# Performance work log

Hardware: AMD Instinct MI355X
Metric: run time of the kernel (lower is better)

Reference implementation:

```python
import math
import jax, jax.numpy as jnp
import numpy as np

B, S, E, H = 2, 2048, 1024, 16
D = E // H  # head_dim = 64
NEG = jnp.float32(-1e9)  # finite stand-in for masked_fill(-inf) to avoid NaN in attn @ V


def setup_inputs() -> dict:
    key = jax.random.key(0)
    ks = jax.random.split(key, 8)
    inp = {
        "query": jax.random.normal(ks[0], (B, S, E), jnp.float32),
        "key": jax.random.normal(ks[1], (B, S, E), jnp.float32),
        "value": jax.random.normal(ks[2], (B, S, E), jnp.float32),
        "Wq": jax.random.normal(ks[3], (E, E), jnp.float32) * 0.02,
        "bq": jnp.zeros((E,), jnp.float32),
        "Wk": jax.random.normal(ks[4], (E, E), jnp.float32) * 0.02,
        "bk": jnp.zeros((E,), jnp.float32),
        "Wv": jax.random.normal(ks[5], (E, E), jnp.float32) * 0.02,
        "bv": jnp.zeros((E,), jnp.float32),
        "pos_bias": jax.random.normal(ks[6], (H, 2 * S - 1), jnp.float32) * 0.02,
    }
    # gather indices: per-head row index [H,1,1] and relative-position index [S,S]
    inp["idx0"] = jnp.arange(H, dtype=jnp.int32).reshape(H, 1, 1)
    rel = np.arange(S)[:, None] - np.arange(S)[None, :] + (S - 1)  # in [0, 2S-2]
    inp["idx1"] = jnp.asarray(rel, jnp.int32)
    # causal boolean mask: True where masked (j > i)
    inp["mask"] = jnp.triu(jnp.ones((S, S), jnp.bool_), k=1)
    return inp


def _split(x):  # [B,S,E] -> [B,H,S,D]
    return x.reshape(B, S, H, D).transpose(0, 2, 1, 3)


def reference(query, key, value, Wq, bq, Wk, bk, Wv, bv, pos_bias, idx0, idx1, mask):
    q = _split(query @ Wq.T + bq)
    k = _split(key @ Wk.T + bk)
    v = _split(value @ Wv.T + bv)
    logits = jnp.einsum("bhqd,bhkd->bhqk", q, k) / math.sqrt(D)  # [B,H,S,S]
    logits = logits + pos_bias[idx0, idx1]  # gather -> [H,S,S], broadcast over B
    logits = jnp.where(mask, NEG, logits)   # masked_fill
    attn = jax.nn.log_softmax(logits, axis=-1)  # module uses LogSoftmax (faithful)
    out = jnp.einsum("bhqk,bhkd->bhqd", attn, v)
    return out.transpose(0, 2, 1, 3).reshape(B, S, E)
```

## Files before the change

kernel.cpp:

```cpp
#include <hip/hip_runtime.h>
#include <math.h>

constexpr int BB = 2;
constexpr int SS = 2048;
constexpr int EE = 1024;
constexpr int HH = 16;
constexpr int DD = 64;

typedef short short8 __attribute__((ext_vector_type(8)));
typedef short short4_t __attribute__((ext_vector_type(4)));
typedef float floatx4 __attribute__((ext_vector_type(4)));
typedef unsigned short ushort_t;

__device__ __forceinline__ ushort_t f2bf(float f) {
    unsigned int u = __float_as_uint(f);
    u += 0x7fffu + ((u >> 16) & 1u);
    return (ushort_t)(u >> 16);
}
__device__ __forceinline__ float bf2f(short s) {
    return __uint_as_float(((unsigned)(ushort_t)s) << 16);
}

__device__ __forceinline__ void gl_lds16(const void* g, void* l) {
    __builtin_amdgcn_global_load_lds(
        (const __attribute__((address_space(1))) void*)g,
        (__attribute__((address_space(3))) void*)l, 16, 0, 0);
}

__global__ __launch_bounds__(256) void repack_all(
    const float* __restrict__ x0, const float* __restrict__ x1, const float* __restrict__ x2,
    const float* __restrict__ w0, const float* __restrict__ w1, const float* __restrict__ w2,
    ushort_t* __restrict__ Xbf, ushort_t* __restrict__ Wbf)
{
    const int idx = blockIdx.x * 256 + threadIdx.x;
    const int row = idx >> 7;
    const int gir = idx & 127;
    const float* src;
    ushort_t* dst;
    int r;
    if (row < 3 * BB * SS) {
        const int z = row >> 12; r = row & (BB * SS - 1);
        src = (z == 0) ? x0 : (z == 1) ? x1 : x2;
        dst = Xbf + (size_t)z * BB * SS * EE;
    } else {
        const int rw = row - 3 * BB * SS;
        const int z = rw >> 10; r = rw & (EE - 1);
        src = (z == 0) ? w0 : (z == 1) ? w1 : w2;
        dst = Wbf + (size_t)z * EE * EE;
    }
    const int blk = gir >> 3, g = gir & 7;
    const int gp = g ^ (r & 7);
    const float* sp = src + (size_t)r * EE + gir * 8;
    float4 a = *(const float4*)sp;
    float4 b = *(const float4*)(sp + 4);
    short8 o;
    o[0] = (short)f2bf(a.x); o[1] = (short)f2bf(a.y); o[2] = (short)f2bf(a.z); o[3] = (short)f2bf(a.w);
    o[4] = (short)f2bf(b.x); o[5] = (short)f2bf(b.y); o[6] = (short)f2bf(b.z); o[7] = (short)f2bf(b.w);
    *(short8*)&dst[(size_t)r * EE + blk * 64 + gp * 8] = o;
}

__global__ __launch_bounds__(256) void proj_kernel(
    const ushort_t* __restrict__ Xall, const ushort_t* __restrict__ Wall,
    const float* __restrict__ bq, const float* __restrict__ bk, const float* __restrict__ bv,
    ushort_t* __restrict__ qb, ushort_t* __restrict__ kbb, ushort_t* __restrict__ vtb)
{
    __shared__ __align__(16) ushort_t Xs[128 * 64];
    __shared__ __align__(16) ushort_t Ws[128 * 64];

    const int z = blockIdx.z;
    const ushort_t* X = Xall + (size_t)z * BB * SS * EE;
    const ushort_t* W = Wall + (size_t)z * EE * EE;
    const float* bias = (z == 0) ? bq : (z == 1) ? bk : bv;

    const int t = threadIdx.x, w = t >> 6, l = t & 63, ln = t & 15, qd = (t >> 4) & 3;
    const int row0 = blockIdx.x * 128;
    const int col0 = blockIdx.y * 128;
    const int wzm = (w & 1) * 64, wzn = (w >> 1) * 64;

    floatx4 acc[4][4];
    #pragma unroll
    for (int i = 0; i < 4; ++i)
        #pragma unroll
        for (int j = 0; j < 4; ++j)
            acc[i][j] = (floatx4){0.f, 0.f, 0.f, 0.f};

    for (int k0 = 0; k0 < EE; k0 += 64) {
        __syncthreads();
        #pragma unroll
        for (int j = 0; j < 4; ++j) {
            const int c = w * 4 + j;
            const int r = c * 8 + (l >> 3);
            gl_lds16(&X[(size_t)(row0 + r) * EE + k0 + (l & 7) * 8], &Xs[c * 512]);
            gl_lds16(&W[(size_t)(col0 + r) * EE + k0 + (l & 7) * 8], &Ws[c * 512]);
        }
        __syncthreads();

        const ushort_t* Am = (z < 2) ? Ws : Xs;
        const ushort_t* Bn = (z < 2) ? Xs : Ws;
        #pragma unroll
        for (int kh = 0; kh < 2; ++kh) {
            const int sw = ((kh * 4 + qd) ^ (ln & 7)) * 8;
            short8 af[4], bfr[4];
            #pragma unroll
            for (int mi = 0; mi < 4; ++mi)
                af[mi] = *(const short8*)&Am[(wzm + mi * 16 + ln) * 64 + sw];
            #pragma unroll
            for (int ni = 0; ni < 4; ++ni)
                bfr[ni] = *(const short8*)&Bn[(wzn + ni * 16 + ln) * 64 + sw];
            #pragma unroll
            for (int mi = 0; mi < 4; ++mi)
                #pragma unroll
                for (int ni = 0; ni < 4; ++ni)
                    acc[mi][ni] = __builtin_amdgcn_mfma_f32_16x16x32_bf16(af[mi], bfr[ni], acc[mi][ni], 0, 0, 0);
        }
    }

    if (z < 2) {
        ushort_t* dst = z ? kbb : qb;
        #pragma unroll
        for (int mi = 0; mi < 4; ++mi) {
            const int o0 = col0 + wzm + mi * 16 + qd * 4;
            const float4 b4 = *(const float4*)&bias[o0];
            const int h = o0 >> 6, d0 = o0 & 63;
            const int g = d0 >> 3, dlow = d0 & 7;
            #pragma unroll
            for (int ni = 0; ni < 4; ++ni) {
                const int s = row0 + wzn + ni * 16 + ln;
                const int b = s >> 11, sr = s & (SS - 1);
                const int gp = g ^ (sr & 7);
                short4_t pk;
                pk[0] = (short)f2bf(acc[mi][ni][0] + b4.x);
                pk[1] = (short)f2bf(acc[mi][ni][1] + b4.y);
                pk[2] = (short)f2bf(acc[mi][ni][2] + b4.z);
                pk[3] = (short)f2bf(acc[mi][ni][3] + b4.w);
                *(short4_t*)&dst[((size_t)((b * HH + h) * SS) + sr) * DD + gp * 8 + dlow] = pk;
            }
        }
    } else {
        #pragma unroll
        for (int mi = 0; mi < 4; ++mi) {
            const int s0 = row0 + wzm + mi * 16 + qd * 4;
            const int b = s0 >> 11, sr0 = s0 & (SS - 1);
            const int sg = (sr0 >> 3) & 7, slow = sr0 & 7;
            #pragma unroll
            for (int ni = 0; ni < 4; ++ni) {
                const int o = col0 + wzn + ni * 16 + ln;
                const int h = o >> 6, d = o & 63;
                const float bvv = bias[o];
                const int gp2 = sg ^ (d & 7);
                short4_t pk;
                pk[0] = (short)f2bf(acc[mi][ni][0] + bvv);
                pk[1] = (short)f2bf(acc[mi][ni][1] + bvv);
                pk[2] = (short)f2bf(acc[mi][ni][2] + bvv);
                pk[3] = (short)f2bf(acc[mi][ni][3] + bvv);
                *(short4_t*)&vtb[((size_t)((b * HH + h) * DD) + d) * SS + (sr0 & ~63) + gp2 * 8 + slow] = pk;
            }
        }
    }
}

__global__ __launch_bounds__(256) void scan_chunks(
    const ushort_t* __restrict__ vtb, float* __restrict__ segsuf)
{
    const int t = threadIdx.x;
    const int d = blockIdx.x * 8 + (t >> 5);
    const int ch = t & 31;
    const int bh = blockIdx.y;
    const ushort_t* src = vtb + ((size_t)(bh * DD + d)) * SS + ch * 64;
    float s = 0.f;
    #pragma unroll
    for (int i = 0; i < 8; ++i) {
        short8 v = *(const short8*)&src[i * 8];
        #pragma unroll
        for (int j = 0; j < 8; ++j) s += bf2f(v[j]);
    }
    #pragma unroll
    for (int delta = 1; delta < 32; delta <<= 1) {
        const float v = __shfl_down(s, delta, 32);
        if (ch + delta < 32) s += v;
    }
    segsuf[((size_t)bh * 33 + ch) * 64 + d] = s;
    if (ch == 31) segsuf[((size_t)bh * 33 + 32) * 64 + d] = 0.f;
}

__global__ __launch_bounds__(256, 4) void attn_kernel(
    const ushort_t* __restrict__ qb, const ushort_t* __restrict__ kbb,
    const ushort_t* __restrict__ vtb, const float* __restrict__ segsuf,
    const float* __restrict__ pb, float* __restrict__ out)
{
    __shared__ float pbL[2048];

    const int t = threadIdx.x, w = t >> 6, ln = t & 15, qd = (t >> 4) & 3;

    const int id = blockIdx.x;
    const int r_ = id & 255, g_ = id >> 8;
    const int bh = r_ & 31, tq = r_ >> 5;
    const int qt = (g_ == 0) ? (31 - tq)
                 : (g_ == 1) ? (23 - tq)
                 : (g_ == 2) ? (8 + tq) : tq;
    const int b = bh >> 4, h = bh & 15, i0 = qt * 64;
    const int r0 = 16 * w;

    {
        const float* p = pb + h * (2 * SS - 1) + (SS - 1);
        #pragma unroll
        for (int j = 0; j < 8; ++j) pbL[t * 8 + j] = p[t * 8 + j];
    }
    __syncthreads();

    const ushort_t* Kbh = kbb + (size_t)bh * SS * DD;
    const ushort_t* Vbh = vtb + (size_t)bh * DD * SS;

    short8 qf[2];
    #pragma unroll
    for (int kh = 0; kh < 2; ++kh)
        qf[kh] = *(const short8*)&qb[((size_t)bh * SS + i0 + r0 + ln) * DD + (((kh * 4 + qd) ^ (ln & 7)) * 8)];

    floatx4 accpv[4], accsv[4];
    #pragma unroll
    for (int ct = 0; ct < 4; ++ct) {
        accpv[ct] = (floatx4){0.f, 0.f, 0.f, 0.f};
        accsv[ct] = (floatx4){0.f, 0.f, 0.f, 0.f};
    }
    float psum0 = 0.f, psum1 = 0.f;

    for (int kt = 0; kt < qt; ++kt) {
        const int k0 = kt * 64;

        floatx4 aq[4];
        #pragma unroll
        for (int mt = 0; mt < 4; ++mt) aq[mt] = (floatx4){0.f, 0.f, 0.f, 0.f};
        #pragma unroll
        for (int kh = 0; kh < 2; ++kh) {
            const int sw = ((kh * 4 + qd) ^ (ln & 7)) * 8;
            #pragma unroll
            for (int mt = 0; mt < 4; ++mt) {
                short8 af = *(const short8*)&Kbh[(size_t)(k0 + mt * 16 + ln) * DD + sw];
                aq[mt] = __builtin_amdgcn_mfma_f32_16x16x32_bf16(af, qf[kh], aq[mt], 0, 0, 0);
            }
        }

        short4_t pfrag[4];
        const int base0 = i0 - k0 + r0 + ln;
        #pragma unroll
        for (int mt = 0; mt < 4; ++mt) {
            const int base = base0 - mt * 16 - qd * 4;
            #pragma unroll
            for (int reg = 0; reg < 4; ++reg) {
                const float val = aq[mt][reg] * 0.125f + pbL[base - reg];
                if (reg & 1) psum1 += __expf(val); else psum0 += __expf(val);
                pfrag[mt][reg] = (short)f2bf(val);
            }
        }

        #pragma unroll
        for (int kk = 0; kk < 4; ++kk) {
            #pragma unroll
            for (int ct = 0; ct < 4; ++ct) {
                const size_t off = (size_t)(ct * 16 + ln) * SS + k0
                                 + ((((kk * 2 + (qd >> 1)) ^ (ln & 7)) * 8) + (qd & 1) * 4);
                short4_t bfr = *(const short4_t*)&Vbh[off];
                accpv[ct] = __builtin_amdgcn_mfma_f32_16x16x16bf16_1k(pfrag[kk], bfr, accpv[ct], 0, 0, 0);
            }
        }
    }

    {
        const int k0 = qt * 64;
        const int iloc = r0 + ln;

        floatx4 aq[4];
        #pragma unroll
        for (int mt = 0; mt < 4; ++mt) aq[mt] = (floatx4){0.f, 0.f, 0.f, 0.f};
        #pragma unroll
        for (int kh = 0; kh < 2; ++kh) {
            const int sw = ((kh * 4 + qd) ^ (ln & 7)) * 8;
            #pragma unroll
            for (int mt = 0; mt < 4; ++mt) {
                short8 af = *(const short8*)&Kbh[(size_t)(k0 + mt * 16 + ln) * DD + sw];
                aq[mt] = __builtin_amdgcn_mfma_f32_16x16x32_bf16(af, qf[kh], aq[mt], 0, 0, 0);
            }
        }

        short4_t pfrag[4];
        #pragma unroll
        for (int mt = 0; mt < 4; ++mt) {
            const int base = r0 + ln - mt * 16 - qd * 4;
            #pragma unroll
            for (int reg = 0; reg < 4; ++reg) {
                const int rel = base - reg;
                const bool ok = rel >= 0;
                const float val = aq[mt][reg] * 0.125f + pbL[ok ? rel : 0];
                psum0 += ok ? __expf(val) : 0.f;
                pfrag[mt][reg] = ok ? (short)f2bf(val) : (short)0;
            }
        }

        #pragma unroll
        for (int kk = 0; kk < 4; ++kk) {
            short4_t uf;
            #pragma unroll
            for (int j = 0; j < 4; ++j)
                uf[j] = (kk * 16 + qd * 4 + j > iloc) ? (short)0x3F80 : (short)0;
            #pragma unroll
            for (int ct = 0; ct < 4; ++ct) {
                const size_t off = (size_t)(ct * 16 + ln) * SS + k0
                                 + ((((kk * 2 + (qd >> 1)) ^ (ln & 7)) * 8) + (qd & 1) * 4);
                short4_t bfr = *(const short4_t*)&Vbh[off];
                accpv[ct] = __builtin_amdgcn_mfma_f32_16x16x16bf16_1k(pfrag[kk], bfr, accpv[ct], 0, 0, 0);
                accsv[ct] = __builtin_amdgcn_mfma_f32_16x16x16bf16_1k(uf, bfr, accsv[ct], 0, 0, 0);
            }
        }
    }

    float p = psum0 + psum1;
    p += __shfl_xor(p, 16, 64);
    p += __shfl_xor(p, 32, 64);
    const float lseq = __logf(p);
    float lseR[4];
    #pragma unroll
    for (int reg = 0; reg < 4; ++reg)
        lseR[reg] = __shfl(lseq, qd * 4 + reg, 64);

    const int cmin = qt + 1;
    float tot[4], tail[4];
    #pragma unroll
    for (int ct = 0; ct < 4; ++ct) {
        const int d = ct * 16 + ln;
        tot[ct]  = segsuf[((size_t)bh * 33) * 64 + d];
        tail[ct] = segsuf[((size_t)bh * 33 + cmin) * 64 + d];
    }

    #pragma unroll
    for (int ct = 0; ct < 4; ++ct) {
        const int d = ct * 16 + ln;
        #pragma unroll
        for (int reg = 0; reg < 4; ++reg) {
            const int ig = i0 + r0 + qd * 4 + reg;
            const float o = accpv[ct][reg] - lseR[reg] * tot[ct]
                          - 1e9f * (accsv[ct][reg] + tail[ct]);
            out[((size_t)(b * SS + ig)) * EE + h * DD + d] = o;
        }
    }
}

extern "C" void kernel_launch(void* const* d_in, const int* in_sizes, int n_in,
                              void* d_out, int out_size, void* d_ws, size_t ws_size,
                              hipStream_t stream)
{
    const float* query = (const float*)d_in[0];
    const float* key_  = (const float*)d_in[1];
    const float* value = (const float*)d_in[2];
    const float* Wq = (const float*)d_in[3];
    const float* bq = (const float*)d_in[4];
    const float* Wk = (const float*)d_in[5];
    const float* bk = (const float*)d_in[6];
    const float* Wv = (const float*)d_in[7];
    const float* bv = (const float*)d_in[8];
    const float* pb = (const float*)d_in[9];
    float* out = (float*)d_out;

    float* ws = (float*)d_ws;
    const size_t SZ = (size_t)BB * SS * EE;
    float* segsuf = ws;
    ushort_t* us  = (ushort_t*)(segsuf + (size_t)BB * HH * 33 * DD);
    ushort_t* qbp = us;
    ushort_t* kbp = qbp + SZ;
    ushort_t* vtp = kbp + SZ;
    ushort_t* Xbf = vtp + SZ;
    ushort_t* Wbf = Xbf + 3 * SZ;

    const int ngroups = (3 * BB * SS + 3 * EE) * (EE / 8);
    repack_all<<<ngroups / 256, 256, 0, stream>>>(query, key_, value, Wq, Wk, Wv, Xbf, Wbf);

    proj_kernel<<<dim3(BB * SS / 128, EE / 128, 3), 256, 0, stream>>>(
        Xbf, Wbf, bq, bk, bv, qbp, kbp, vtp);

    scan_chunks<<<dim3(8, BB * HH), 256, 0, stream>>>(vtp, segsuf);

    attn_kernel<<<BB * HH * (SS / 64), 256, 0, stream>>>(
        qbp, kbp, vtp, segsuf, pb, out);
}
```

Before: 270.8 us.

## Stage K and V tiles into double-buffered LDS with async global-to-LDS loads

The attention loop used to read K and transposed V straight from global memory inside the MFMA loops. It now copies each 64-key tile of K and V into double-buffered shared memory with global_load_lds, prefetching the next tile while the current one is computed, and uses explicit vmcnt waits and barriers. The diagonal tile is folded into the same loop under a flag. This adds 32KB of LDS per block, which may lower occupancy against launch_bounds(256,4), and adds two barriers per iteration.

```diff
diff --git a/kernel.cpp b/kernel.cpp
--- a/kernel.cpp
+++ b/kernel.cpp
@@ -188,6 +188,8 @@
     const ushort_t* __restrict__ vtb, const float* __restrict__ segsuf,
     const float* __restrict__ pb, float* __restrict__ out)
 {
+    __shared__ __align__(16) ushort_t Ks[2][64 * 64];
+    __shared__ __align__(16) ushort_t Vt[2][64 * 64];
     __shared__ float pbL[2048];
 
     const int t = threadIdx.x, w = t >> 6, ln = t & 15, qd = (t >> 4) & 3;
@@ -201,20 +203,31 @@
     const int b = bh >> 4, h = bh & 15, i0 = qt * 64;
     const int r0 = 16 * w;
 
+    const ushort_t* Kbh = kbb + (size_t)bh * SS * DD;
+    const ushort_t* Vbh = vtb + (size_t)bh * DD * SS;
+
+    const int srow = t >> 3, scg = t & 7;
+    auto stage = [&](int buf, int kt) {
+        const int k0 = kt * 64;
+        gl_lds16(&Kbh[(size_t)(k0 + srow) * DD + scg * 8],      &Ks[buf][w * 512]);
+        gl_lds16(&Kbh[(size_t)(k0 + 32 + srow) * DD + scg * 8], &Ks[buf][2048 + w * 512]);
+        gl_lds16(&Vbh[(size_t)srow * SS + k0 + scg * 8],        &Vt[buf][w * 512]);
+        gl_lds16(&Vbh[(size_t)(32 + srow) * SS + k0 + scg * 8], &Vt[buf][2048 + w * 512]);
+    };
+
     {
         const float* p = pb + h * (2 * SS - 1) + (SS - 1);
         #pragma unroll
         for (int j = 0; j < 8; ++j) pbL[t * 8 + j] = p[t * 8 + j];
     }
-    __syncthreads();
-
-    const ushort_t* Kbh = kbb + (size_t)bh * SS * DD;
-    const ushort_t* Vbh = vtb + (size_t)bh * DD * SS;
 
     short8 qf[2];
     #pragma unroll
     for (int kh = 0; kh < 2; ++kh)
         qf[kh] = *(const short8*)&qb[((size_t)bh * SS + i0 + r0 + ln) * DD + (((kh * 4 + qd) ^ (ln & 7)) * 8)];
+
+    stage(0, 0);
+    __syncthreads();
 
     floatx4 accpv[4], accsv[4];
     #pragma unroll
@@ -224,8 +237,20 @@
     }
     float psum0 = 0.f, psum1 = 0.f;
 
-    for (int kt = 0; kt < qt; ++kt) {
+    for (int kt = 0; kt <= qt; ++kt) {
         const int k0 = kt * 64;
+        const bool diag = (kt == qt);
+
+        if (!diag) {
+            stage((kt + 1) & 1, kt + 1);
+            asm volatile("s_waitcnt vmcnt(4)" ::: "memory");
+        } else {
+            asm volatile("s_waitcnt vmcnt(0)" ::: "memory");
+        }
+        __builtin_amdgcn_s_barrier();
+
+        const ushort_t* KsC = Ks[kt & 1];
+        const ushort_t* VtC = Vt[kt & 1];
 
         floatx4 aq[4];
         #pragma unroll
@@ -235,82 +260,60 @@
             const int sw = ((kh * 4 + qd) ^ (ln & 7)) * 8;
             #pragma unroll
             for (int mt = 0; mt < 4; ++mt) {
-                short8 af = *(const short8*)&Kbh[(size_t)(k0 + mt * 16 + ln) * DD + sw];
+                short8 af = *(const short8*)&KsC[(mt * 16 + ln) * 64 + sw];
                 aq[mt] = __builtin_amdgcn_mfma_f32_16x16x32_bf16(af, qf[kh], aq[mt], 0, 0, 0);
             }
         }
 
         short4_t pfrag[4];
-        const int base0 = i0 - k0 + r0 + ln;
-        #pragma unroll
-        for (int mt = 0; mt < 4; ++mt) {
-            const int base = base0 - mt * 16 - qd * 4;
-            #pragma unroll
-            for (int reg = 0; reg < 4; ++reg) {
-                const float val = aq[mt][reg] * 0.125f + pbL[base - reg];
-                if (reg & 1) psum1 += __expf(val); else psum0 += __expf(val);
-                pfrag[mt][reg] = (short)f2bf(val);
-            }
-        }
-
-        #pragma unroll
-        for (int kk = 0; kk < 4; ++kk) {
-            #pragma unroll
-            for (int ct = 0; ct < 4; ++ct) {
-                const size_t off = (size_t)(ct * 16 + ln) * SS + k0
-                                 + ((((kk * 2 + (qd >> 1)) ^ (ln & 7)) * 8) + (qd & 1) * 4);
-                short4_t bfr = *(const short4_t*)&Vbh[off];
-                accpv[ct] = __builtin_amdgcn_mfma_f32_16x16x16bf16_1k(pfrag[kk], bfr, accpv[ct], 0, 0, 0);
-            }
-        }
-    }
-
-    {
-        const int k0 = qt * 64;
+        if (!diag) {
+            const int base0 = i0 - k0 + r0 + ln;
+            #pragma unroll
+            for (int mt = 0; mt < 4; ++mt) {
+                const int base = base0 - mt * 16 - qd * 4;
+                #pragma unroll
+                for (int reg = 0; reg < 4; ++reg) {
+                    const float val = aq[mt][reg] * 0.125f + pbL[base - reg];
+                    if (reg & 1) psum1 += __expf(val); else psum0 += __expf(val);
+                    pfrag[mt][reg] = (short)f2bf(val);
+                }
+            }
+        } else {
+            #pragma unroll
+            for (int mt = 0; mt < 4; ++mt) {
+                const int base = r0 + ln - mt * 16 - qd * 4;
+                #pragma unroll
+                for (int reg = 0; reg < 4; ++reg) {
+                    const int rel = base - reg;
+                    const bool ok = rel >= 0;
+                    const float val = aq[mt][reg] * 0.125f + pbL[ok ? rel : 0];
+                    psum0 += ok ? __expf(val) : 0.f;
+                    pfrag[mt][reg] = ok ? (short)f2bf(val) : (short)0;
+                }
+            }
+        }
+
         const int iloc = r0 + ln;
-
-        floatx4 aq[4];
-        #pragma unroll
-        for (int mt = 0; mt < 4; ++mt) aq[mt] = (floatx4){0.f, 0.f, 0.f, 0.f};
-        #pragma unroll
-        for (int kh = 0; kh < 2; ++kh) {
-            const int sw = ((kh * 4 + qd) ^ (ln & 7)) * 8;
-            #pragma unroll
-            for (int mt = 0; mt < 4; ++mt) {
-                short8 af = *(const short8*)&Kbh[(size_t)(k0 + mt * 16 + ln) * DD + sw];
-                aq[mt] = __builtin_amdgcn_mfma_f32_16x16x32_bf16(af, qf[kh], aq[mt], 0, 0, 0);
-            }
-        }
-
-        short4_t pfrag[4];
-        #pragma unroll
-        for (int mt = 0; mt < 4; ++mt) {
-            const int base = r0 + ln - mt * 16 - qd * 4;
-            #pragma unroll
-            for (int reg = 0; reg < 4; ++reg) {
-                const int rel = base - reg;
-                const bool ok = rel >= 0;
-                const float val = aq[mt][reg] * 0.125f + pbL[ok ? rel : 0];
-                psum0 += ok ? __expf(val) : 0.f;
-                pfrag[mt][reg] = ok ? (short)f2bf(val) : (short)0;
-            }
-        }
-
         #pragma unroll
         for (int kk = 0; kk < 4; ++kk) {
             short4_t uf;
-            #pragma unroll
-            for (int j = 0; j < 4; ++j)
-                uf[j] = (kk * 16 + qd * 4 + j > iloc) ? (short)0x3F80 : (short)0;
+            if (diag) {
+                #pragma unroll
+                for (int j = 0; j < 4; ++j)
+                    uf[j] = (kk * 16 + qd * 4 + j > iloc) ? (short)0x3F80 : (short)0;
+            }
             #pragma unroll
             for (int ct = 0; ct < 4; ++ct) {
-                const size_t off = (size_t)(ct * 16 + ln) * SS + k0
-                                 + ((((kk * 2 + (qd >> 1)) ^ (ln & 7)) * 8) + (qd & 1) * 4);
-                short4_t bfr = *(const short4_t*)&Vbh[off];
+                const int off = (ct * 16 + ln) * 64 + (((kk * 2 + (qd >> 1)) ^ (ln & 7)) * 8 + (qd & 1) * 4);
+                short4_t bfr = *(const short4_t*)&VtC[off];
                 accpv[ct] = __builtin_amdgcn_mfma_f32_16x16x16bf16_1k(pfrag[kk], bfr, accpv[ct], 0, 0, 0);
-                accsv[ct] = __builtin_amdgcn_mfma_f32_16x16x16bf16_1k(uf, bfr, accsv[ct], 0, 0, 0);
-            }
-        }
+                if (diag)
+                    accsv[ct] = __builtin_amdgcn_mfma_f32_16x16x16bf16_1k(uf, bfr, accsv[ct], 0, 0, 0);
+            }
+        }
+
+        if (!diag)
+            __builtin_amdgcn_s_barrier();
     }
 
     float p = psum0 + psum1;
```

Result: faster. 231.2 us (-14.6%).
